# Performance work log

Hardware: AMD Instinct MI355X
Metric: run time of the kernel (lower is better)

Reference implementation:

```python
import jax, jax.numpy as jnp
import numpy as np

B, T, C, H, M, O = 64, 2048, 256, 512, 512, 256
EPS = 1e-12


def retract(x):
    # Unit-sphere retraction: project onto the sphere (stand-in for the abstract Manifold).
    return x * jax.lax.rsqrt(jnp.sum(x * x, axis=-1, keepdims=True) + EPS)


def setup_inputs() -> dict:
    key = jax.random.key(0)
    ks = jax.random.split(key, 12)
    s = lambda k, shape, fan: jax.random.normal(k, shape, jnp.float32) / np.sqrt(fan).astype(np.float32)
    return {
        "control_values": jax.random.normal(ks[0], (B, T, C), jnp.float32),
        # initial-condition MLP (depth=2: in->M->M->H, softplus between hidden layers)
        "mlp_w0": s(ks[1], (M, C), C), "mlp_b0": jnp.zeros((M,), jnp.float32),
        "mlp_w1": s(ks[2], (M, M), M), "mlp_b1": jnp.zeros((M,), jnp.float32),
        "mlp_w2": s(ks[3], (H, M), M), "mlp_b2": jnp.zeros((H,), jnp.float32),
        # eqx.nn.GRUCell params
        "w_ih": s(ks[4], (3 * H, C), C), "w_hh": s(ks[5], (3 * H, H), H),
        "b": s(ks[6], (3 * H,), H), "b_n": s(ks[7], (H,), H),
        # readout Linear
        "w_out": s(ks[8], (O, H), H), "b_out": jnp.zeros((O,), jnp.float32),
    }


def reference(control_values, mlp_w0, mlp_b0, mlp_w1, mlp_b1, mlp_w2, mlp_b2,
              w_ih, w_hh, b, b_n, w_out, b_out):
    # Initial hidden state from MLP on x[0], then hidden-manifold retract.
    x0 = control_values[:, 0]                                  # (B, C)
    h = jax.nn.softplus(x0 @ mlp_w0.T + mlp_b0)                # (B, M)
    h = jax.nn.softplus(h @ mlp_w1.T + mlp_b1)                 # (B, M)
    h0 = retract(h @ mlp_w2.T + mlp_b2)                        # (B, H)

    xs = jnp.transpose(control_values[:, 1:], (1, 0, 2))       # (T-1, B, C)

    def step(hprev, xt):
        ig = xt @ w_ih.T + b                                   # (B, 3H)
        hg = hprev @ w_hh.T                                    # (B, 3H)
        ir, iz, inn = jnp.split(ig, 3, axis=-1)
        hr, hz, hn = jnp.split(hg, 3, axis=-1)
        r = jax.nn.sigmoid(ir + hr)
        z = jax.nn.sigmoid(iz + hz)
        n = jnp.tanh(inn + r * (hn + b_n))
        hnew = retract(n + z * (hprev - n))                    # GRU update + manifold retract
        return hnew, hnew

    _, hs_rest = jax.lax.scan(step, h0, xs)                    # (T-1, B, H)
    hs = jnp.concatenate([h0[None], hs_rest], axis=0)          # (T, B, H)

    # evolving_out=True: readout (identity activation) + manifold retract per step.
    y = retract(hs @ w_out.T + b_out)                          # (T, B, O)
    return jnp.transpose(y, (1, 0, 2))                         # (B, T, O)
```

## Files before the change

kernel.cpp:

```cpp
#include <hip/hip_runtime.h>
#include <math.h>

#define B_  64
#define T_  2048
#define C_  256
#define H_  512
#define O_  256
#define NSTEP 2047

typedef __attribute__((ext_vector_type(8))) short short8x;
typedef __attribute__((ext_vector_type(4))) float f32x4;

__device__ __forceinline__ unsigned short f2bf_bits(float x){
  unsigned int u = __builtin_bit_cast(unsigned int, x);
  u = u + 0x7FFFu + ((u >> 16) & 1u);
  return (unsigned short)(u >> 16);
}
__device__ __forceinline__ float bf2f(unsigned short h){
  unsigned int u = ((unsigned int)h) << 16;
  return __builtin_bit_cast(float, u);
}
__device__ __forceinline__ short8x pack8(float4 a, float4 b){
  short8x w;
  w[0]=(short)f2bf_bits(a.x); w[1]=(short)f2bf_bits(a.y);
  w[2]=(short)f2bf_bits(a.z); w[3]=(short)f2bf_bits(a.w);
  w[4]=(short)f2bf_bits(b.x); w[5]=(short)f2bf_bits(b.y);
  w[6]=(short)f2bf_bits(b.z); w[7]=(short)f2bf_bits(b.w);
  return w;
}
__device__ __forceinline__ f32x4 MFMA(short8x a, short8x b, f32x4 c){
  return __builtin_amdgcn_mfma_f32_16x16x32_bf16(a, b, c, 0, 0, 0);
}
__device__ __forceinline__ float softplus_f(float x){
  return (x > 20.f) ? x : log1pf(expf(x));
}
__device__ __forceinline__ float fast_exp2(float x){ return __builtin_amdgcn_exp2f(x); }
__device__ __forceinline__ float fast_rcp(float x){ return __builtin_amdgcn_rcpf(x); }
__device__ __forceinline__ float sigmoid_f(float x){
  return fast_rcp(1.f + fast_exp2(-1.44269504f * x));
}
__device__ __forceinline__ float tanh_f(float x){
  return 1.f - 2.f * fast_rcp(1.f + fast_exp2(2.88539008f * x));
}

__device__ __forceinline__ void st_agent_u16(unsigned short* p, unsigned short v){
  __hip_atomic_store(p, v, __ATOMIC_RELAXED, __HIP_MEMORY_SCOPE_AGENT);
}
__device__ __forceinline__ unsigned long long ld_agent_u64(unsigned long long* p){
  return __hip_atomic_load(p, __ATOMIC_RELAXED, __HIP_MEMORY_SCOPE_AGENT);
}

__device__ __forceinline__ int has_ffff(unsigned long long w){
  unsigned long long nv = ~w;
  return ((nv - 0x0001000100010001ull) & ~nv & 0x8000800080008000ull) != 0ull;
}
__device__ __forceinline__ float sq4(unsigned long long w){
  unsigned lo = (unsigned)w, hi = (unsigned)(w >> 32);
  float f0 = __builtin_bit_cast(float, lo << 16);
  float f1 = __builtin_bit_cast(float, lo & 0xFFFF0000u);
  float f2 = __builtin_bit_cast(float, hi << 16);
  float f3 = __builtin_bit_cast(float, hi & 0xFFFF0000u);
  return f0*f0 + f1*f1 + f2*f2 + f3*f3;
}
__device__ __forceinline__ short8x to8(unsigned long long w0, unsigned long long w1){
  union { unsigned long long q[2]; short8x s; } u;
  u.q[0] = w0; u.q[1] = w1;
  return u.s;
}

__device__ __forceinline__ void barrier_lds(){
  asm volatile("s_waitcnt lgkmcnt(0)" ::: "memory");
  __builtin_amdgcn_s_barrier();
  asm volatile("" ::: "memory");
}
__device__ __forceinline__ void barrier_exec(){
  asm volatile("" ::: "memory");
  __builtin_amdgcn_s_barrier();
  asm volatile("" ::: "memory");
}


__global__ void k_mlp(const float* __restrict__ cv,
                      const float* __restrict__ w0, const float* __restrict__ bb0,
                      const float* __restrict__ w1, const float* __restrict__ bb1,
                      const float* __restrict__ w2, const float* __restrict__ bb2,
                      unsigned short* __restrict__ hs)
{
  const int b = blockIdx.x, tid = threadIdx.x;
  const int wave = tid >> 6, lane = tid & 63;
  __shared__ float xr[256], a0[512], a1[512], a2[512];

  xr[tid] = cv[(size_t)b * T_ * C_ + tid];
  __syncthreads();

  for (int i = 0; i < 32; i++){
    float s[4];
    #pragma unroll
    for (int uu = 0; uu < 4; uu++){
      int j = wave*128 + i*4 + uu;
      const float4* wr = (const float4*)(w0 + (size_t)j * 256);
      float4 w = wr[lane];
      s[uu] = w.x*xr[lane*4+0] + w.y*xr[lane*4+1] + w.z*xr[lane*4+2] + w.w*xr[lane*4+3];
    }
    #pragma unroll
    for (int off = 32; off; off >>= 1){
      #pragma unroll
      for (int uu = 0; uu < 4; uu++) s[uu] += __shfl_xor(s[uu], off, 64);
    }
    if (lane < 4){ int j = wave*128 + i*4 + lane; a0[j] = softplus_f(s[lane] + bb0[j]); }
  }
  __syncthreads();

  for (int i = 0; i < 32; i++){
    float s[4];
    #pragma unroll
    for (int uu = 0; uu < 4; uu++){
      int j = wave*128 + i*4 + uu;
      const float4* wr = (const float4*)(w1 + (size_t)j * 512);
      float4 wA = wr[lane*2], wB = wr[lane*2+1];
      int k0 = lane*8;
      s[uu] = wA.x*a0[k0]   + wA.y*a0[k0+1] + wA.z*a0[k0+2] + wA.w*a0[k0+3]
            + wB.x*a0[k0+4] + wB.y*a0[k0+5] + wB.z*a0[k0+6] + wB.w*a0[k0+7];
    }
    #pragma unroll
    for (int off = 32; off; off >>= 1){
      #pragma unroll
      for (int uu = 0; uu < 4; uu++) s[uu] += __shfl_xor(s[uu], off, 64);
    }
    if (lane < 4){ int j = wave*128 + i*4 + lane; a1[j] = softplus_f(s[lane] + bb1[j]); }
  }
  __syncthreads();

  for (int i = 0; i < 32; i++){
    float s[4];
    #pragma unroll
    for (int uu = 0; uu < 4; uu++){
      int j = wave*128 + i*4 + uu;
      const float4* wr = (const float4*)(w2 + (size_t)j * 512);
      float4 wA = wr[lane*2], wB = wr[lane*2+1];
      int k0 = lane*8;
      s[uu] = wA.x*a1[k0]   + wA.y*a1[k0+1] + wA.z*a1[k0+2] + wA.w*a1[k0+3]
            + wB.x*a1[k0+4] + wB.y*a1[k0+5] + wB.z*a1[k0+6] + wB.w*a1[k0+7];
    }
    #pragma unroll
    for (int off = 32; off; off >>= 1){
      #pragma unroll
      for (int uu = 0; uu < 4; uu++) s[uu] += __shfl_xor(s[uu], off, 64);
    }
    if (lane < 4){ int j = wave*128 + i*4 + lane; a2[j] = s[lane] + bb2[j]; }
  }
  __syncthreads();

  const int g = b >> 4, bb = b & 15;
  {
    int u = tid;
    hs[(size_t)g*8192 + (u>>5)*512 + bb*32 + (u&31)] = f2bf_bits(a2[u]);
    u = tid + 256;
    hs[(size_t)g*8192 + (u>>5)*512 + bb*32 + (u&31)] = f2bf_bits(a2[u]);
  }
}

__global__ void k_wcvt(const float* __restrict__ w, unsigned short* __restrict__ o)
{
  int idx = blockIdx.x * 256 + threadIdx.x;
  if (idx < O_ * H_) o[idx] = f2bf_bits(w[idx]);
}

__global__ __launch_bounds__(256, 1)
void k_scan(const float* __restrict__ cv, const float* __restrict__ w_ih,
            const float* __restrict__ w_hh, const float* __restrict__ bias,
            const float* __restrict__ b_n,
            unsigned short* __restrict__ hs, float* __restrict__ sumsq)
{
  const int wg   = blockIdx.x;
  const int g    = wg >> 4;
  const int sidx = wg & 15;
  const int b0   = g * 16;
  const int u0   = sidx * 32;
  const int tid  = threadIdx.x;
  const int wave = tid >> 6, lane = tid & 63;
  const int lm   = lane & 15, quad = lane >> 4;
  const int gb   = tid >> 5;
  const int uu   = tid & 31;

  __shared__ float accLds[12][16][16];
  __shared__ float ssq[3][16];
  __shared__ float bias_lds[3][32];
  __shared__ float bn_lds[32];

  if (tid < 32){
    bias_lds[0][tid] = bias[u0 + tid];
    bias_lds[1][tid] = bias[512 + u0 + tid];
    bias_lds[2][tid] = bias[1024 + u0 + tid];
    bn_lds[tid]      = b_n[u0 + tid];
  }
  float hp0 = bf2f(hs[(size_t)g*8192 + sidx*512 + gb*32 + uu]);
  float hp1 = bf2f(hs[(size_t)g*8192 + sidx*512 + (gb+8)*32 + uu]);

  short8x wreg[48];
  if (wave < 3){
    const int gate = wave;
    #pragma unroll
    for (int nt = 0; nt < 2; nt++){
      #pragma unroll
      for (int k = 0; k < 16; k++){
        const float* p = w_hh + ((size_t)(gate*512 + u0 + nt*16 + lm)) * 512 + k*32 + quad*8;
        wreg[nt*16 + k] = pack8(*(const float4*)p, *(const float4*)(p + 4));
      }
    }
  } else {
    #pragma unroll
    for (int g2 = 0; g2 < 3; g2++){
      #pragma unroll
      for (int nt = 0; nt < 2; nt++){
        #pragma unroll
        for (int kk = 0; kk < 8; kk++){
          const float* p = w_ih + ((size_t)(g2*512 + u0 + nt*16 + lm)) * 256 + kk*32 + quad*8;
          wreg[(g2*2 + nt)*8 + kk] = pack8(*(const float4*)p, *(const float4*)(p + 4));
        }
      }
    }
  }
  __syncthreads();

  for (int t = 1; t <= NSTEP; t++){
    if (wave < 3){
      unsigned long long* base =
        (unsigned long long*)(hs + ((size_t)(t-1)*4 + g)*8192 + lm*32 + quad*8);
      unsigned long long v0[16], v1[16];
      unsigned pend = 0xFFFFu;
      do {
        #pragma unroll
        for (int k = 0; k < 16; k++){
          if (pend & (1u<<k)){
            v0[k] = ld_agent_u64(base + (size_t)k*128);
            v1[k] = ld_agent_u64(base + (size_t)k*128 + 1);
          }
        }
        unsigned np = 0u;
        #pragma unroll
        for (int k = 0; k < 16; k++){
          if ((pend & (1u<<k)) && (has_ffff(v0[k]) | has_ffff(v1[k]))) np |= (1u<<k);
        }
        pend = np;
      } while (__any((int)pend));

      f32x4 acc0 = {0.f,0.f,0.f,0.f}, acc1 = {0.f,0.f,0.f,0.f};
      #pragma unroll
      for (int k = 0; k < 16; k++){
        short8x a = to8(v0[k], v1[k]);
        acc0 = MFMA(a, wreg[k],      acc0);
        acc1 = MFMA(a, wreg[16 + k], acc1);
      }
      #pragma unroll
      for (int r = 0; r < 4; r++){
        accLds[wave*2 + 0][quad*4 + r][lm] = acc0[r];
        accLds[wave*2 + 1][quad*4 + r][lm] = acc1[r];
      }

      const int klo = (wave == 0) ? 0 : (wave == 1 ? 6 : 11);
      const int khi = (wave == 0) ? 6 : (wave == 1 ? 11 : 16);
      float s = 0.f;
      #pragma unroll
      for (int k = 0; k < 16; k++){
        if (k >= klo && k < khi) s += sq4(v0[k]) + sq4(v1[k]);
      }
      s += __shfl_xor(s, 16, 64);
      s += __shfl_xor(s, 32, 64);
      if (lane < 16) ssq[wave][lane] = s;
    } else {
      short8x af[8];
      const size_t xbase = ((size_t)(b0 + lm) * T_ + t) * C_;
      #pragma unroll
      for (int kk = 0; kk < 8; kk++){
        const float* xp = cv + xbase + kk*32 + quad*8;
        af[kk] = pack8(*(const float4*)xp, *(const float4*)(xp + 4));
      }
      f32x4 acc[6];
      #pragma unroll
      for (int tt = 0; tt < 6; tt++) acc[tt] = (f32x4){0.f,0.f,0.f,0.f};
      #pragma unroll
      for (int kk = 0; kk < 8; kk++){
        #pragma unroll
        for (int tt = 0; tt < 6; tt++) acc[tt] = MFMA(af[kk], wreg[tt*8 + kk], acc[tt]);
      }
      #pragma unroll
      for (int tt = 0; tt < 6; tt++){
        #pragma unroll
        for (int r = 0; r < 4; r++) accLds[6 + tt][quad*4 + r][lm] = acc[tt][r];
      }
    }
    barrier_lds();

    const int nt = uu >> 4, ul = uu & 15;
    const float s0 = ssq[0][gb]   + ssq[1][gb]   + ssq[2][gb];
    const float s1 = ssq[0][gb+8] + ssq[1][gb+8] + ssq[2][gb+8];
    if (sidx == 0 && uu == 0){
      sumsq[(size_t)(t-1)*64 + b0 + gb]     = s0;
      sumsq[(size_t)(t-1)*64 + b0 + gb + 8] = s1;
    }
    {
      const float sp = rsqrtf(s0 + 1e-12f);
      float rv = accLds[6 + 0 + nt][gb][ul] + bias_lds[0][uu] + sp*accLds[0 + nt][gb][ul];
      float zv = accLds[6 + 2 + nt][gb][ul] + bias_lds[1][uu] + sp*accLds[2 + nt][gb][ul];
      float nv = accLds[6 + 4 + nt][gb][ul] + bias_lds[2][uu];
      float hn = sp*accLds[4 + nt][gb][ul];
      float r  = sigmoid_f(rv);
      float z  = sigmoid_f(zv);
      float n  = tanh_f(nv + r*(hn + bn_lds[uu]));
      float hp = sp * hp0;
      float hnew = n + z*(hp - n);
      hp0 = hnew;
      st_agent_u16(hs + ((size_t)t*4 + g)*8192 + sidx*512 + gb*32 + uu, f2bf_bits(hnew));
    }
    {
      const float sp = rsqrtf(s1 + 1e-12f);
      float rv = accLds[6 + 0 + nt][gb+8][ul] + bias_lds[0][uu] + sp*accLds[0 + nt][gb+8][ul];
      float zv = accLds[6 + 2 + nt][gb+8][ul] + bias_lds[1][uu] + sp*accLds[2 + nt][gb+8][ul];
      float nv = accLds[6 + 4 + nt][gb+8][ul] + bias_lds[2][uu];
      float hn = sp*accLds[4 + nt][gb+8][ul];
      float r  = sigmoid_f(rv);
      float z  = sigmoid_f(zv);
      float n  = tanh_f(nv + r*(hn + bn_lds[uu]));
      float hp = sp * hp1;
      float hnew = n + z*(hp - n);
      hp1 = hnew;
      st_agent_u16(hs + ((size_t)t*4 + g)*8192 + sidx*512 + (gb+8)*32 + uu, f2bf_bits(hnew));
    }
    barrier_exec();
  }

  if (sidx == 0 && wave == 0){
    unsigned long long* base =
      (unsigned long long*)(hs + ((size_t)NSTEP*4 + g)*8192 + lm*32 + quad*8);
    unsigned long long v0[16], v1[16];
    unsigned pend = 0xFFFFu;
    do {
      #pragma unroll
      for (int k = 0; k < 16; k++){
        if (pend & (1u<<k)){
          v0[k] = ld_agent_u64(base + (size_t)k*128);
          v1[k] = ld_agent_u64(base + (size_t)k*128 + 1);
        }
      }
      unsigned np = 0u;
      #pragma unroll
      for (int k = 0; k < 16; k++){
        if ((pend & (1u<<k)) && (has_ffff(v0[k]) | has_ffff(v1[k]))) np |= (1u<<k);
      }
      pend = np;
    } while (__any((int)pend));
    float s = 0.f;
    #pragma unroll
    for (int k = 0; k < 16; k++) s += sq4(v0[k]) + sq4(v1[k]);
    s += __shfl_xor(s, 16, 64);
    s += __shfl_xor(s, 32, 64);
    if (lane < 16) sumsq[(size_t)NSTEP*64 + b0 + lane] = s;
  }
}

__global__ __launch_bounds__(256, 2)
void k_ygemm(const unsigned short* __restrict__ hs, const float* __restrict__ sumsq,
             const unsigned short* __restrict__ wob, const float* __restrict__ b_out,
             float* __restrict__ out)
{
  const int t = blockIdx.x;
  const int tid = threadIdx.x, wave = tid >> 6, lane = tid & 63;
  const int lm = lane & 15, quad = lane >> 4;
  __shared__ float srow[64];
  __shared__ float bo[256];
  __shared__ float part[4][64];
  __shared__ float ysc[64];

  if (tid < 64) srow[tid] = rsqrtf(sumsq[(size_t)t*64 + tid] + 1e-12f);
  bo[tid] = b_out[tid];
  __syncthreads();

  f32x4 acc[4][4];
  #pragma unroll
  for (int mt = 0; mt < 4; mt++)
    #pragma unroll
    for (int nt = 0; nt < 4; nt++) acc[mt][nt] = (f32x4){0.f,0.f,0.f,0.f};

  const unsigned short* arow[4];
  const unsigned short* brow[4];
  #pragma unroll
  for (int mt = 0; mt < 4; mt++)
    arow[mt] = hs + ((size_t)t*4 + mt)*8192 + lm*32 + quad*8;
  #pragma unroll
  for (int nt = 0; nt < 4; nt++)
    brow[nt] = wob + ((size_t)(wave*64 + nt*16 + lm))*512 + quad*8;

  #pragma unroll 2
  for (int k = 0; k < 16; k++){
    short8x a[4], b[4];
    #pragma unroll
    for (int mt = 0; mt < 4; mt++) a[mt] = *(const short8x*)(arow[mt] + (size_t)k*512);
    #pragma unroll
    for (int nt = 0; nt < 4; nt++) b[nt] = *(const short8x*)(brow[nt] + k*32);
    #pragma unroll
    for (int mt = 0; mt < 4; mt++)
      #pragma unroll
      for (int nt = 0; nt < 4; nt++) acc[mt][nt] = MFMA(a[mt], b[nt], acc[mt][nt]);
  }

  float loc[4][4];
  #pragma unroll
  for (int mt = 0; mt < 4; mt++)
    #pragma unroll
    for (int r = 0; r < 4; r++) loc[mt][r] = 0.f;
  #pragma unroll
  for (int mt = 0; mt < 4; mt++){
    #pragma unroll
    for (int nt = 0; nt < 4; nt++){
      f32x4 v = acc[mt][nt];
      #pragma unroll
      for (int r = 0; r < 4; r++){
        int row = mt*16 + quad*4 + r;
        float y = srow[row]*v[r] + bo[wave*64 + nt*16 + lm];
        v[r] = y;
        loc[mt][r] += y*y;
      }
      acc[mt][nt] = v;
    }
  }
  #pragma unroll
  for (int off = 8; off; off >>= 1){
    #pragma unroll
    for (int mt = 0; mt < 4; mt++)
      #pragma unroll
      for (int r = 0; r < 4; r++) loc[mt][r] += __shfl_xor(loc[mt][r], off, 16);
  }
  if (lm == 0){
    #pragma unroll
    for (int mt = 0; mt < 4; mt++)
      #pragma unroll
      for (int r = 0; r < 4; r++) part[wave][mt*16 + quad*4 + r] = loc[mt][r];
  }
  __syncthreads();
  if (tid < 64) ysc[tid] = rsqrtf(part[0][tid] + part[1][tid] + part[2][tid] + part[3][tid] + 1e-12f);
  __syncthreads();

  #pragma unroll
  for (int mt = 0; mt < 4; mt++){
    #pragma unroll
    for (int nt = 0; nt < 4; nt++){
      #pragma unroll
      for (int r = 0; r < 4; r++){
        int row = mt*16 + quad*4 + r;
        int o   = wave*64 + nt*16 + lm;
        out[((size_t)row * T_ + t) * O_ + o] = acc[mt][nt][r] * ysc[row];
      }
    }
  }
}

extern "C" void kernel_launch(void* const* d_in, const int* in_sizes, int n_in,
                              void* d_out, int out_size, void* d_ws, size_t ws_size,
                              hipStream_t stream)
{
  (void)in_sizes; (void)n_in; (void)out_size;
  const float* cv   = (const float*)d_in[0];
  const float* w0   = (const float*)d_in[1];
  const float* b0v  = (const float*)d_in[2];
  const float* w1   = (const float*)d_in[3];
  const float* b1v  = (const float*)d_in[4];
  const float* w2   = (const float*)d_in[5];
  const float* b2v  = (const float*)d_in[6];
  const float* wih  = (const float*)d_in[7];
  const float* whh  = (const float*)d_in[8];
  const float* bg   = (const float*)d_in[9];
  const float* bn   = (const float*)d_in[10];
  const float* wout = (const float*)d_in[11];
  const float* bout = (const float*)d_in[12];
  float* out = (float*)d_out;

  const size_t HS_BYTES  = (size_t)T_ * B_ * H_ * 2;
  const size_t SS_BYTES  = (size_t)T_ * B_ * 4;
  const size_t OFF_SS    = HS_BYTES;
  const size_t OFF_WOB   = OFF_SS + SS_BYTES;
  const size_t NEED      = OFF_WOB + (size_t)O_ * H_ * 2;
  if (ws_size < NEED) return;

  unsigned short* hs    = (unsigned short*)d_ws;
  float*          sumsq = (float*)((char*)d_ws + OFF_SS);
  unsigned short* wob   = (unsigned short*)((char*)d_ws + OFF_WOB);

  const size_t T0_BYTES = (size_t)4 * 8192 * 2;
  hipMemsetAsync((char*)d_ws + T0_BYTES, 0xFF, HS_BYTES - T0_BYTES, stream);

  hipLaunchKernelGGL(k_mlp,   dim3(64),   dim3(256), 0, stream,
                     cv, w0, b0v, w1, b1v, w2, b2v, hs);
  hipLaunchKernelGGL(k_wcvt,  dim3(512),  dim3(256), 0, stream, wout, wob);
  hipLaunchKernelGGL(k_scan,  dim3(64),   dim3(256), 0, stream,
                     cv, wih, whh, bg, bn, hs, sumsq);
  hipLaunchKernelGGL(k_ygemm, dim3(2048), dim3(256), 0, stream,
                     hs, sumsq, wob, bout, out);
}
```

Baseline: 9.036 ms.

## Distribute hidden-state polling across all waves via LDS tile and prefetch next step

Instead of three waves each polling all 16 hidden-state chunks from global memory, each of the four waves polls three or four remote chunks and stages them into a shared LDS tile. The workgroup's own chunk is written locally and never polled. The next step's loads are issued right after the current step's stores, and x-projection inputs are loaded before the spin-wait. Stores are packed into 32-bit atomics and the own-chunk sum of squares is computed locally. This cuts redundant global polling and latency on the serial recurrence critical path, at the cost of an extra LDS barrier per step and more complex synchronization.

```diff
diff --git a/kernel.cpp b/kernel.cpp
--- a/kernel.cpp
+++ b/kernel.cpp
@@ -43,7 +43,7 @@
   return 1.f - 2.f * fast_rcp(1.f + fast_exp2(2.88539008f * x));
 }
 
-__device__ __forceinline__ void st_agent_u16(unsigned short* p, unsigned short v){
+__device__ __forceinline__ void st_agent_u32(unsigned* p, unsigned v){
   __hip_atomic_store(p, v, __ATOMIC_RELAXED, __HIP_MEMORY_SCOPE_AGENT);
 }
 __device__ __forceinline__ unsigned long long ld_agent_u64(unsigned long long* p){
@@ -79,6 +79,9 @@
   asm volatile("" ::: "memory");
 }
 
+__device__ __forceinline__ size_t chunk_off(int t, int g, int c, int lm, int quad){
+  return ((size_t)t*4 + g)*8192 + (size_t)c*512 + lm*32 + quad*8;
+}
 
 __global__ void k_mlp(const float* __restrict__ cv,
                       const float* __restrict__ w0, const float* __restrict__ bb0,
@@ -183,8 +186,10 @@
   const int gb   = tid >> 5;
   const int uu   = tid & 31;
 
+  __shared__ unsigned short tileS[16*512];
   __shared__ float accLds[12][16][16];
-  __shared__ float ssq[3][16];
+  __shared__ float ssqR[4][16];
+  __shared__ float ssqOwn[2][16];
   __shared__ float bias_lds[3][32];
   __shared__ float bn_lds[32];
 
@@ -221,34 +226,76 @@
       }
     }
   }
+
+  const int CH = (wave < 3) ? 4 : 3;
+  int cs[4];
+  #pragma unroll
+  for (int s = 0; s < 4; s++){ int j = wave*4 + s; cs[s] = j + (j >= sidx ? 1 : 0); }
+
+  tileS[sidx*512 + gb*32 + uu]     = f2bf_bits(hp0);
+  tileS[sidx*512 + (gb+8)*32 + uu] = f2bf_bits(hp1);
+  {
+    float sq0 = hp0*hp0, sq1 = hp1*hp1;
+    #pragma unroll
+    for (int off = 16; off; off >>= 1){
+      sq0 += __shfl_down(sq0, off, 32);
+      sq1 += __shfl_down(sq1, off, 32);
+    }
+    if ((lane & 31) == 0){ ssqOwn[0][gb] = sq0; ssqOwn[0][gb+8] = sq1; }
+  }
+  unsigned long long vv[8];
+  unsigned pend = (1u << CH) - 1u;
+  #pragma unroll
+  for (int s = 0; s < 4; s++) if (s < CH){
+    unsigned long long* p = (unsigned long long*)(hs + chunk_off(0, g, cs[s], lm, quad));
+    vv[2*s]   = ld_agent_u64(p);
+    vv[2*s+1] = ld_agent_u64(p + 1);
+  }
   __syncthreads();
 
   for (int t = 1; t <= NSTEP; t++){
+    short8x af3[8];
+    if (wave == 3){
+      const size_t xbase = ((size_t)(b0 + lm) * T_ + t) * C_;
+      #pragma unroll
+      for (int kk = 0; kk < 8; kk++){
+        const float* xp = cv + xbase + kk*32 + quad*8;
+        af3[kk] = pack8(*(const float4*)xp, *(const float4*)(xp + 4));
+      }
+    }
+    while (pend){
+      unsigned np = 0u;
+      #pragma unroll
+      for (int s = 0; s < 4; s++)
+        if (s < CH && ((pend >> s) & 1u) && (has_ffff(vv[2*s]) | has_ffff(vv[2*s+1])))
+          np |= 1u << s;
+      pend = np;
+      if (!pend) break;
+      #pragma unroll
+      for (int s = 0; s < 4; s++) if (s < CH && ((pend >> s) & 1u)){
+        unsigned long long* p = (unsigned long long*)(hs + chunk_off(t-1, g, cs[s], lm, quad));
+        vv[2*s]   = ld_agent_u64(p);
+        vv[2*s+1] = ld_agent_u64(p + 1);
+      }
+    }
+    {
+      float sq = 0.f;
+      #pragma unroll
+      for (int s = 0; s < 4; s++) if (s < CH){
+        *(short8x*)&tileS[cs[s]*512 + lm*32 + quad*8] = to8(vv[2*s], vv[2*s+1]);
+        sq += sq4(vv[2*s]) + sq4(vv[2*s+1]);
+      }
+      sq += __shfl_xor(sq, 16, 64);
+      sq += __shfl_xor(sq, 32, 64);
+      if (lane < 16) ssqR[wave][lane] = sq;
+    }
+    barrier_lds();
+
     if (wave < 3){
-      unsigned long long* base =
-        (unsigned long long*)(hs + ((size_t)(t-1)*4 + g)*8192 + lm*32 + quad*8);
-      unsigned long long v0[16], v1[16];
-      unsigned pend = 0xFFFFu;
-      do {
-        #pragma unroll
-        for (int k = 0; k < 16; k++){
-          if (pend & (1u<<k)){
-            v0[k] = ld_agent_u64(base + (size_t)k*128);
-            v1[k] = ld_agent_u64(base + (size_t)k*128 + 1);
-          }
-        }
-        unsigned np = 0u;
-        #pragma unroll
-        for (int k = 0; k < 16; k++){
-          if ((pend & (1u<<k)) && (has_ffff(v0[k]) | has_ffff(v1[k]))) np |= (1u<<k);
-        }
-        pend = np;
-      } while (__any((int)pend));
-
       f32x4 acc0 = {0.f,0.f,0.f,0.f}, acc1 = {0.f,0.f,0.f,0.f};
       #pragma unroll
       for (int k = 0; k < 16; k++){
-        short8x a = to8(v0[k], v1[k]);
+        short8x a = *(const short8x*)&tileS[k*512 + lm*32 + quad*8];
         acc0 = MFMA(a, wreg[k],      acc0);
         acc1 = MFMA(a, wreg[16 + k], acc1);
       }
@@ -257,32 +304,14 @@
         accLds[wave*2 + 0][quad*4 + r][lm] = acc0[r];
         accLds[wave*2 + 1][quad*4 + r][lm] = acc1[r];
       }
-
-      const int klo = (wave == 0) ? 0 : (wave == 1 ? 6 : 11);
-      const int khi = (wave == 0) ? 6 : (wave == 1 ? 11 : 16);
-      float s = 0.f;
-      #pragma unroll
-      for (int k = 0; k < 16; k++){
-        if (k >= klo && k < khi) s += sq4(v0[k]) + sq4(v1[k]);
-      }
-      s += __shfl_xor(s, 16, 64);
-      s += __shfl_xor(s, 32, 64);
-      if (lane < 16) ssq[wave][lane] = s;
     } else {
-      short8x af[8];
-      const size_t xbase = ((size_t)(b0 + lm) * T_ + t) * C_;
-      #pragma unroll
-      for (int kk = 0; kk < 8; kk++){
-        const float* xp = cv + xbase + kk*32 + quad*8;
-        af[kk] = pack8(*(const float4*)xp, *(const float4*)(xp + 4));
-      }
       f32x4 acc[6];
       #pragma unroll
       for (int tt = 0; tt < 6; tt++) acc[tt] = (f32x4){0.f,0.f,0.f,0.f};
       #pragma unroll
       for (int kk = 0; kk < 8; kk++){
         #pragma unroll
-        for (int tt = 0; tt < 6; tt++) acc[tt] = MFMA(af[kk], wreg[tt*8 + kk], acc[tt]);
+        for (int tt = 0; tt < 6; tt++) acc[tt] = MFMA(af3[kk], wreg[tt*8 + kk], acc[tt]);
       }
       #pragma unroll
       for (int tt = 0; tt < 6; tt++){
@@ -292,13 +321,15 @@
     }
     barrier_lds();
 
-    const int nt = uu >> 4, ul = uu & 15;
-    const float s0 = ssq[0][gb]   + ssq[1][gb]   + ssq[2][gb];
-    const float s1 = ssq[0][gb+8] + ssq[1][gb+8] + ssq[2][gb+8];
+    const int par = (t - 1) & 1;
+    const float s0 = ssqR[0][gb]   + ssqR[1][gb]   + ssqR[2][gb]   + ssqR[3][gb]   + ssqOwn[par][gb];
+    const float s1 = ssqR[0][gb+8] + ssqR[1][gb+8] + ssqR[2][gb+8] + ssqR[3][gb+8] + ssqOwn[par][gb+8];
     if (sidx == 0 && uu == 0){
       sumsq[(size_t)(t-1)*64 + b0 + gb]     = s0;
       sumsq[(size_t)(t-1)*64 + b0 + gb + 8] = s1;
     }
+    const int nt = uu >> 4, ul = uu & 15;
+    float hnew0, hnew1;
     {
       const float sp = rsqrtf(s0 + 1e-12f);
       float rv = accLds[6 + 0 + nt][gb][ul] + bias_lds[0][uu] + sp*accLds[0 + nt][gb][ul];
@@ -309,9 +340,8 @@
       float z  = sigmoid_f(zv);
       float n  = tanh_f(nv + r*(hn + bn_lds[uu]));
       float hp = sp * hp0;
-      float hnew = n + z*(hp - n);
-      hp0 = hnew;
-      st_agent_u16(hs + ((size_t)t*4 + g)*8192 + sidx*512 + gb*32 + uu, f2bf_bits(hnew));
+      hnew0 = n + z*(hp - n);
+      hp0 = hnew0;
     }
     {
       const float sp = rsqrtf(s1 + 1e-12f);
@@ -323,10 +353,40 @@
       float z  = sigmoid_f(zv);
       float n  = tanh_f(nv + r*(hn + bn_lds[uu]));
       float hp = sp * hp1;
-      float hnew = n + z*(hp - n);
-      hp1 = hnew;
-      st_agent_u16(hs + ((size_t)t*4 + g)*8192 + sidx*512 + (gb+8)*32 + uu, f2bf_bits(hnew));
-    }
+      hnew1 = n + z*(hp - n);
+      hp1 = hnew1;
+    }
+    unsigned short bb0 = f2bf_bits(hnew0), bb1 = f2bf_bits(hnew1);
+    tileS[sidx*512 + gb*32 + uu]     = bb0;
+    tileS[sidx*512 + (gb+8)*32 + uu] = bb1;
+    {
+      unsigned n0 = __shfl_xor((unsigned)bb0, 1, 64);
+      unsigned n1 = __shfl_xor((unsigned)bb1, 1, 64);
+      if (!(uu & 1)){
+        unsigned* q0 = (unsigned*)(hs + ((size_t)t*4 + g)*8192 + sidx*512 + gb*32 + uu);
+        unsigned* q1 = (unsigned*)(hs + ((size_t)t*4 + g)*8192 + sidx*512 + (gb+8)*32 + uu);
+        st_agent_u32(q0, (unsigned)bb0 | (n0 << 16));
+        st_agent_u32(q1, (unsigned)bb1 | (n1 << 16));
+      }
+    }
+    {
+      float sq0 = hnew0*hnew0, sq1 = hnew1*hnew1;
+      #pragma unroll
+      for (int off = 16; off; off >>= 1){
+        sq0 += __shfl_down(sq0, off, 32);
+        sq1 += __shfl_down(sq1, off, 32);
+      }
+      if ((lane & 31) == 0){ ssqOwn[t & 1][gb] = sq0; ssqOwn[t & 1][gb+8] = sq1; }
+    }
+    if (t < NSTEP){
+      pend = (1u << CH) - 1u;
+      #pragma unroll
+      for (int s = 0; s < 4; s++) if (s < CH){
+        unsigned long long* p = (unsigned long long*)(hs + chunk_off(t, g, cs[s], lm, quad));
+        vv[2*s]   = ld_agent_u64(p);
+        vv[2*s+1] = ld_agent_u64(p + 1);
+      }
+    } else pend = 0u;
     barrier_exec();
   }
 
@@ -334,11 +394,11 @@
     unsigned long long* base =
       (unsigned long long*)(hs + ((size_t)NSTEP*4 + g)*8192 + lm*32 + quad*8);
     unsigned long long v0[16], v1[16];
-    unsigned pend = 0xFFFFu;
+    unsigned pend2 = 0xFFFFu;
     do {
       #pragma unroll
       for (int k = 0; k < 16; k++){
-        if (pend & (1u<<k)){
+        if (pend2 & (1u<<k)){
           v0[k] = ld_agent_u64(base + (size_t)k*128);
           v1[k] = ld_agent_u64(base + (size_t)k*128 + 1);
         }
@@ -346,10 +406,10 @@
       unsigned np = 0u;
       #pragma unroll
       for (int k = 0; k < 16; k++){
-        if ((pend & (1u<<k)) && (has_ffff(v0[k]) | has_ffff(v1[k]))) np |= (1u<<k);
-      }
-      pend = np;
-    } while (__any((int)pend));
+        if ((pend2 & (1u<<k)) && (has_ffff(v0[k]) | has_ffff(v1[k]))) np |= (1u<<k);
+      }
+      pend2 = np;
+    } while (__any((int)pend2));
     float s = 0.f;
     #pragma unroll
     for (int k = 0; k < 16; k++) s += sq4(v0[k]) + sq4(v1[k]);
```

Result: slower. 13.04 ms (+44.3%).
